# Optimization experiments

Hardware: AMD Instinct MI355X
Metric: run time of the kernel (lower is better)

Reference implementation:

```python
import jax, jax.numpy as jnp
import numpy as np

DIM = 768
HEADS = 12
HEAD_DIM = DIM // HEADS
HIDDEN = 4 * DIM
SCALE = HEAD_DIM ** -0.5
LN_EPS = 1e-5


def _fit_poly_gelu():
    # replicate PolyGELU.__init__: quadratic least-squares fit to exact GELU on [-3,3]
    x = np.linspace(-3.0, 3.0, 10000).astype(np.float32)
    y = np.asarray(jax.nn.gelu(jnp.asarray(x), approximate=False))
    X = np.stack([x ** 2, x, np.ones_like(x)], axis=1)
    c, *_ = np.linalg.lstsq(X, y, rcond=None)
    return c.astype(np.float32)  # [a, b, c]


def setup_inputs() -> dict:
    key = jax.random.key(0)
    ks = jax.random.split(key, 8)
    g = _fit_poly_gelu()
    w = lambda k, shp: (jax.random.normal(k, shp, dtype=jnp.float32) * 0.02)
    return {
        "x": jax.random.normal(ks[0], (4, 2048, DIM), dtype=jnp.float32),
        "ln1_g": jnp.ones((DIM,), jnp.float32),
        "ln1_b": jnp.zeros((DIM,), jnp.float32),
        "ln2_g": jnp.ones((DIM,), jnp.float32),
        "ln2_b": jnp.zeros((DIM,), jnp.float32),
        "qkv_w": w(ks[1], (DIM, 3 * DIM)),   # stored [in, out]
        "qkv_b": jnp.zeros((3 * DIM,), jnp.float32),
        "proj_w": w(ks[2], (DIM, DIM)),
        "proj_b": jnp.zeros((DIM,), jnp.float32),
        "fc1_w": w(ks[3], (DIM, HIDDEN)),
        "fc1_b": jnp.zeros((HIDDEN,), jnp.float32),
        "fc2_w": w(ks[4], (HIDDEN, DIM)),
        "fc2_b": jnp.zeros((DIM,), jnp.float32),
        "attn_a": jnp.float32(0.05),
        "attn_b": jnp.float32(0.5),
        "attn_c": jnp.float32(0.25),
        "gelu_a": jnp.float32(g[0]),
        "gelu_b": jnp.float32(g[1]),
        "gelu_c": jnp.float32(g[2]),
    }


def _layernorm(x, gamma, beta):
    mu = jnp.mean(x, axis=-1, keepdims=True)
    var = jnp.mean(jnp.square(x - mu), axis=-1, keepdims=True)
    return (x - mu) / jnp.sqrt(var + LN_EPS) * gamma + beta


def reference(x, ln1_g, ln1_b, ln2_g, ln2_b, qkv_w, qkv_b, proj_w, proj_b,
              fc1_w, fc1_b, fc2_w, fc2_b, attn_a, attn_b, attn_c,
              gelu_a, gelu_b, gelu_c):
    B, N, C = x.shape
    # --- attention branch ---
    h = _layernorm(x, ln1_g, ln1_b)
    qkv = (h @ qkv_w + qkv_b).reshape(B, N, 3, HEADS, HEAD_DIM)
    q, k, v = (qkv[:, :, i].transpose(0, 2, 1, 3) for i in range(3))  # [B,H,N,D]
    attn = jnp.einsum("bhnd,bhmd->bhnm", q, k) * SCALE
    # poly_normed: quadratic activation, clamp, row-normalize
    attn = attn_a * attn * attn + attn_b * attn + attn_c
    attn = jnp.maximum(attn, 1e-6)
    attn = attn / (jnp.sum(attn, axis=-1, keepdims=True) + 1e-8)
    out = jnp.einsum("bhnm,bhmd->bhnd", attn, v).transpose(0, 2, 1, 3).reshape(B, N, C)
    x = x + (out @ proj_w + proj_b)
    # --- MLP branch with PolyGELU ---
    h = _layernorm(x, ln2_g, ln2_b)
    u = h @ fc1_w + fc1_b
    u = gelu_a * u * u + gelu_b * u + gelu_c
    x = x + (u @ fc2_w + fc2_b)
    return x
```

## Files before the change

### kernel.cpp

```cpp
#include <hip/hip_runtime.h>

typedef __bf16 bf16x8 __attribute__((ext_vector_type(8)));
typedef __bf16 bf16x4 __attribute__((ext_vector_type(4)));
typedef float f32x4 __attribute__((ext_vector_type(4)));

#define LN_EPS 1e-5f

__device__ __forceinline__ void gl2lds16(const void* g, void* l) {
  __builtin_amdgcn_global_load_lds(
      (const __attribute__((address_space(1))) unsigned int*)g,
      (__attribute__((address_space(3))) unsigned int*)l, 16, 0, 0);
}

__global__ __launch_bounds__(256) void transpose_k(const float* __restrict__ in,
                                                   __bf16* __restrict__ out,
                                                   int R, int C) {
  __shared__ __bf16 t[32][33];
  int tx = threadIdx.x & 31, ty = threadIdx.x >> 5;
  int c = blockIdx.x * 32 + tx;
  for (int j = 0; j < 4; j++) {
    int r = blockIdx.y * 32 + ty + j * 8;
    t[ty + j * 8][tx] = (__bf16)in[(size_t)r * C + c];
  }
  __syncthreads();
  int r2 = blockIdx.y * 32 + tx;
  for (int j = 0; j < 4; j++) {
    int c2 = blockIdx.x * 32 + ty + j * 8;
    out[(size_t)c2 * R + r2] = t[tx][ty + j * 8];
  }
}

__global__ __launch_bounds__(256) void transpose_v(const __bf16* __restrict__ qkv,
                                                   __bf16* __restrict__ vt) {
  __shared__ __bf16 t[32][33];
  int bh = blockIdx.z;
  int b = bh / 12, h = bh % 12;
  int n0 = blockIdx.x * 32, d0 = blockIdx.y * 32;
  int tx = threadIdx.x & 31, ty = threadIdx.x >> 5;
  for (int j = 0; j < 4; j++) {
    int n = n0 + ty + j * 8;
    t[ty + j * 8][tx] = qkv[(size_t)(b * 2048 + n) * 2304 + 1536 + h * 64 + d0 + tx];
  }
  __syncthreads();
  for (int j = 0; j < 4; j++) {
    int d = d0 + ty + j * 8;
    vt[((size_t)bh * 64 + d) * 2048 + n0 + tx] = t[tx][ty + j * 8];
  }
}

__global__ __launch_bounds__(256) void ln_kernel(const float* __restrict__ x,
                                                 const float* __restrict__ g,
                                                 const float* __restrict__ bta,
                                                 __bf16* __restrict__ out) {
  int row = blockIdx.x;
  size_t base = (size_t)row * 768;
  int t = threadIdx.x;
  float v[3];
  float s = 0.f, s2 = 0.f;
  for (int k = 0; k < 3; k++) {
    float f = x[base + t + k * 256];
    v[k] = f;
    s += f;
    s2 += f * f;
  }
  for (int m = 1; m < 64; m <<= 1) {
    s += __shfl_xor(s, m, 64);
    s2 += __shfl_xor(s2, m, 64);
  }
  __shared__ float sm[4][2];
  int wid = t >> 6, lane = t & 63;
  if (lane == 0) { sm[wid][0] = s; sm[wid][1] = s2; }
  __syncthreads();
  s = sm[0][0] + sm[1][0] + sm[2][0] + sm[3][0];
  s2 = sm[0][1] + sm[1][1] + sm[2][1] + sm[3][1];
  float mu = s * (1.f / 768.f);
  float var = s2 * (1.f / 768.f) - mu * mu;
  float rstd = rsqrtf(var + LN_EPS);
  for (int k = 0; k < 3; k++) {
    int c = t + k * 256;
    out[base + c] = (__bf16)((v[k] - mu) * rstd * g[c] + bta[c]);
  }
}

template <int NT, int EPI>
__global__ __launch_bounds__(256, (NT == 128 ? 3 : 2))
void gemm_bk64(const __bf16* __restrict__ A, const __bf16* __restrict__ BT,
               const float* __restrict__ bias, const float* __restrict__ res,
               void* __restrict__ outv, int M, int N, int K,
               const float* __restrict__ c0p, const float* __restrict__ c1p,
               const float* __restrict__ c2p) {
  __shared__ __bf16 As[128][64];
  __shared__ __bf16 Bs[NT][64];
  const int tid = threadIdx.x, lane = tid & 63, wid = tid >> 6;
  const int wr = wid >> 1, wc = wid & 1;
  const int mr = lane & 15, quad = lane >> 4;
  const int m0 = blockIdx.y * 128, n0 = blockIdx.x * NT;
  const int swzsrc = (((lane & 7) ^ ((lane >> 3) & 7)) * 8);
  const int srow8 = lane >> 3;
  const int col0 = ((quad ^ (mr & 7)) * 8);
  const int col1 = (((4 + quad) ^ (mr & 7)) * 8);

  f32x4 acc[4][NT / 32] = {};

  for (int k0 = 0; k0 < K; k0 += 64) {
    for (int g = 0; g < 4; g++) {
      int r0 = wid * 32 + g * 8 + srow8;
      gl2lds16(&A[(size_t)(m0 + r0) * K + k0 + swzsrc], &As[r0][(lane & 7) * 8]);
    }
    for (int g = 0; g < NT / 32; g++) {
      int r0 = wid * (NT / 4) + g * 8 + srow8;
      gl2lds16(&BT[(size_t)(n0 + r0) * K + k0 + swzsrc], &Bs[r0][(lane & 7) * 8]);
    }
    __syncthreads();
    for (int kk = 0; kk < 2; kk++) {
      const int ck = kk ? col1 : col0;
      bf16x8 af[4], bfr[NT / 32];
      for (int i = 0; i < 4; i++) af[i] = *(bf16x8*)&As[wr * 64 + i * 16 + mr][ck];
      for (int j = 0; j < NT / 32; j++)
        bfr[j] = *(bf16x8*)&Bs[wc * (NT / 2) + j * 16 + mr][ck];
      for (int i = 0; i < 4; i++)
        for (int j = 0; j < NT / 32; j++)
          acc[i][j] = __builtin_amdgcn_mfma_f32_16x16x32_bf16(af[i], bfr[j], acc[i][j], 0, 0, 0);
    }
    __syncthreads();
  }

  float ga = 0.f, gb = 0.f, gc = 0.f;
  if (EPI == 1) { ga = *c0p; gb = *c1p; gc = *c2p; }

  for (int i = 0; i < 4; i++) {
    for (int j = 0; j < NT / 32; j++) {
      int col = n0 + wc * (NT / 2) + j * 16 + mr;
      float bv = bias[col];
      for (int r = 0; r < 4; r++) {
        int row = m0 + wr * 64 + i * 16 + quad * 4 + r;
        size_t idx = (size_t)row * N + col;
        float c = acc[i][j][r] + bv;
        if (EPI == 0) {
          ((__bf16*)outv)[idx] = (__bf16)c;
        } else if (EPI == 1) {
          float u = (ga * c + gb) * c + gc;
          ((__bf16*)outv)[idx] = (__bf16)u;
        } else {
          ((float*)outv)[idx] = c + res[idx];
        }
      }
    }
  }
}

__global__ __launch_bounds__(256, 3) void attn_poly(const __bf16* __restrict__ qkv,
                                                    const __bf16* __restrict__ vt,
                                                    __bf16* __restrict__ outp,
                                                    const float* __restrict__ ap,
                                                    const float* __restrict__ bp,
                                                    const float* __restrict__ cp) {
  __shared__ __bf16 Ps[4][32][72];
  __shared__ __bf16 Kb[2][64][64];
  __shared__ __bf16 Vb[2][64][64];

  const int tid = threadIdx.x, lane = tid & 63, wid = tid >> 6;
  const int mr = lane & 15, quad = lane >> 4;
  const int q0 = blockIdx.x * 128;
  const int h = blockIdx.y, b = blockIdx.z;
  const int bh = b * 12 + h;
  const size_t baseQ = ((size_t)b * 2048) * 2304 + h * 64;

  const int swzsrc = (((lane & 7) ^ ((lane >> 3) & 7)) * 8);
  const int srow8 = lane >> 3;
  const int colS0 = ((quad ^ (mr & 7)) * 8);
  const int colS1 = (((4 + quad) ^ (mr & 7)) * 8);

  bf16x8 qf[2][2];
  for (int i = 0; i < 2; i++)
    for (int s = 0; s < 2; s++)
      qf[i][s] = *(const bf16x8*)&qkv[baseQ + (size_t)(q0 + wid * 32 + i * 16 + mr) * 2304 +
                                      s * 32 + quad * 8];

  const float a2 = (*ap) * 0.015625f, b2 = (*bp) * 0.125f, cc = *cp;
  f32x4 o_acc[2][4] = {};
  float l_acc[2] = {0.f, 0.f};

  auto stage = [&](int kt, int pb) {
    for (int g = 0; g < 2; g++) {
      int r0 = wid * 16 + g * 8 + srow8;
      gl2lds16(&qkv[baseQ + (size_t)(kt * 64 + r0) * 2304 + 768 + swzsrc],
               &Kb[pb][r0][(lane & 7) * 8]);
      gl2lds16(&vt[((size_t)bh * 64 + r0) * 2048 + kt * 64 + swzsrc],
               &Vb[pb][r0][(lane & 7) * 8]);
    }
  };

  stage(0, 0);
  int pb = 0;
  for (int kt = 0; kt < 32; kt++) {
    __syncthreads();
    if (kt < 31) stage(kt + 1, pb ^ 1);

    f32x4 sacc[2][4] = {};
    for (int j = 0; j < 4; j++) {
      for (int s = 0; s < 2; s++) {
        bf16x8 kf = *(bf16x8*)&Kb[pb][j * 16 + mr][s ? colS1 : colS0];
        for (int i = 0; i < 2; i++)
          sacc[i][j] = __builtin_amdgcn_mfma_f32_16x16x32_bf16(kf, qf[i][s], sacc[i][j], 0, 0, 0);
      }
    }
    for (int i = 0; i < 2; i++) {
      f32x4 racc = {0.f, 0.f, 0.f, 0.f};
      for (int j = 0; j < 4; j++) {
        f32x4 S = sacc[i][j];
        f32x4 p = (a2 * S + b2) * S + cc;
        p[0] = fmaxf(p[0], 1e-6f); p[1] = fmaxf(p[1], 1e-6f);
        p[2] = fmaxf(p[2], 1e-6f); p[3] = fmaxf(p[3], 1e-6f);
        racc += p;
        bf16x4 pk = {(__bf16)p[0], (__bf16)p[1], (__bf16)p[2], (__bf16)p[3]};
        *(bf16x4*)&Ps[wid][i * 16 + mr][j * 16 + quad * 4] = pk;
      }
      float rsum = racc[0] + racc[1] + racc[2] + racc[3];
      rsum += __shfl_xor(rsum, 16, 64);
      rsum += __shfl_xor(rsum, 32, 64);
      l_acc[i] += rsum;
    }

    __asm__ __volatile__("s_waitcnt lgkmcnt(0)" ::: "memory");

    for (int s = 0; s < 2; s++) {
      bf16x8 pf[2];
      for (int i = 0; i < 2; i++)
        pf[i] = *(bf16x8*)&Ps[wid][i * 16 + mr][s * 32 + quad * 8];
      for (int dt = 0; dt < 4; dt++) {
        bf16x8 vf = *(bf16x8*)&Vb[pb][dt * 16 + mr][s ? colS1 : colS0];
        for (int i = 0; i < 2; i++)
          o_acc[i][dt] = __builtin_amdgcn_mfma_f32_16x16x32_bf16(pf[i], vf, o_acc[i][dt], 0, 0, 0);
      }
    }
    __asm__ __volatile__("" ::: "memory");
    pb ^= 1;
  }

  size_t baseO = ((size_t)b * 2048) * 768 + h * 64;
  for (int i = 0; i < 2; i++) {
    float inv[4];
    for (int r = 0; r < 4; r++)
      inv[r] = 1.0f / (__shfl(l_acc[i], quad * 4 + r, 64) + 1e-8f);
    for (int dt = 0; dt < 4; dt++) {
      int q = q0 + wid * 32 + i * 16 + quad * 4;
      for (int r = 0; r < 4; r++)
        outp[baseO + (size_t)(q + r) * 768 + dt * 16 + mr] =
            (__bf16)(o_acc[i][dt][r] * inv[r]);
    }
  }
}

extern "C" void kernel_launch(void* const* d_in, const int* in_sizes, int n_in,
                              void* d_out, int out_size, void* d_ws, size_t ws_size,
                              hipStream_t stream) {
  const float* x     = (const float*)d_in[0];
  const float* ln1g  = (const float*)d_in[1];
  const float* ln1b  = (const float*)d_in[2];
  const float* ln2g  = (const float*)d_in[3];
  const float* ln2b  = (const float*)d_in[4];
  const float* qkvw  = (const float*)d_in[5];
  const float* qkvb  = (const float*)d_in[6];
  const float* projw = (const float*)d_in[7];
  const float* projb = (const float*)d_in[8];
  const float* fc1w  = (const float*)d_in[9];
  const float* fc1b  = (const float*)d_in[10];
  const float* fc2w  = (const float*)d_in[11];
  const float* fc2b  = (const float*)d_in[12];
  const float* attna = (const float*)d_in[13];
  const float* attnb = (const float*)d_in[14];
  const float* attnc = (const float*)d_in[15];
  const float* gelua = (const float*)d_in[16];
  const float* gelub = (const float*)d_in[17];
  const float* geluc = (const float*)d_in[18];

  char* ws = (char*)d_ws;
  __bf16* wT_qkv  = (__bf16*)(ws);
  __bf16* wT_proj = (__bf16*)(ws + 3538944);
  __bf16* wT_fc1  = (__bf16*)(ws + 4718592);
  __bf16* wT_fc2  = (__bf16*)(ws + 9437184);
  __bf16* h       = (__bf16*)(ws + 14155776);
  float*  x1      = (float*)(ws + 26738688);
  __bf16* qkvbuf  = (__bf16*)(ws + 51904512);
  __bf16* u       = (__bf16*)(ws + 51904512);
  __bf16* vtbuf   = (__bf16*)(ws + 89653248);
  float*  outp    = (float*)d_out;

  transpose_k<<<dim3(2304 / 32, 768 / 32), 256, 0, stream>>>(qkvw, wT_qkv, 768, 2304);
  transpose_k<<<dim3(768 / 32, 768 / 32), 256, 0, stream>>>(projw, wT_proj, 768, 768);
  transpose_k<<<dim3(3072 / 32, 768 / 32), 256, 0, stream>>>(fc1w, wT_fc1, 768, 3072);
  transpose_k<<<dim3(768 / 32, 3072 / 32), 256, 0, stream>>>(fc2w, wT_fc2, 3072, 768);

  ln_kernel<<<8192, 256, 0, stream>>>(x, ln1g, ln1b, h);
  gemm_bk64<256, 0><<<dim3(9, 64), 256, 0, stream>>>(h, wT_qkv, qkvb, nullptr, qkvbuf,
                                                     8192, 2304, 768, nullptr, nullptr, nullptr);
  transpose_v<<<dim3(64, 2, 48), 256, 0, stream>>>(qkvbuf, vtbuf);
  attn_poly<<<dim3(16, 12, 4), 256, 0, stream>>>(qkvbuf, vtbuf, h, attna, attnb, attnc);
  gemm_bk64<128, 2><<<dim3(6, 64), 256, 0, stream>>>(h, wT_proj, projb, x, x1,
                                                     8192, 768, 768, nullptr, nullptr, nullptr);
  ln_kernel<<<8192, 256, 0, stream>>>(x1, ln2g, ln2b, h);
  gemm_bk64<256, 1><<<dim3(12, 64), 256, 0, stream>>>(h, wT_fc1, fc1b, nullptr, u,
                                                      8192, 3072, 768, gelua, gelub, geluc);
  gemm_bk64<128, 2><<<dim3(6, 64), 256, 0, stream>>>(u, wT_fc2, fc2b, x1, outp,
                                                     8192, 768, 3072, nullptr, nullptr, nullptr);
}
```

Measured before the change: 411.3 us.

## Double-buffer GEMM LDS tiles with BK32 and smaller output tiles

Replaces the single-buffered BK=64 GEMM with a double-buffered BK=32 kernel that issues the next tile's global-to-LDS loads before computing the current one, leaving one barrier per iteration. Tile shapes shrink (128x128 for qkv/fc1, 64x128 for proj/fc2) and occupancy hints rise to 4 blocks per CU, so more blocks fill the GPU. The aim is to hide load latency and raise occupancy, at the cost of less reuse per tile and more K iterations and barriers. The LDS swizzle is changed to a 4-chunk pattern to match the 32-wide rows.

```diff
diff --git a/kernel.cpp b/kernel.cpp
--- a/kernel.cpp
+++ b/kernel.cpp
@@ -82,58 +82,60 @@
   }
 }
 
-template <int NT, int EPI>
-__global__ __launch_bounds__(256, (NT == 128 ? 3 : 2))
-void gemm_bk64(const __bf16* __restrict__ A, const __bf16* __restrict__ BT,
-               const float* __restrict__ bias, const float* __restrict__ res,
-               void* __restrict__ outv, int M, int N, int K,
-               const float* __restrict__ c0p, const float* __restrict__ c1p,
-               const float* __restrict__ c2p) {
-  __shared__ __bf16 As[128][64];
-  __shared__ __bf16 Bs[NT][64];
+template <int MT, int NT, int EPI>
+__global__ __launch_bounds__(256, 4)
+void gemm_db(const __bf16* __restrict__ A, const __bf16* __restrict__ BT,
+             const float* __restrict__ bias, const float* __restrict__ res,
+             void* __restrict__ outv, int M, int N, int K,
+             const float* __restrict__ c0p, const float* __restrict__ c1p,
+             const float* __restrict__ c2p) {
+  __shared__ __bf16 As[2][MT][32];
+  __shared__ __bf16 Bs[2][NT][32];
+  constexpr int IW = MT / 32, JW = NT / 32;
   const int tid = threadIdx.x, lane = tid & 63, wid = tid >> 6;
   const int wr = wid >> 1, wc = wid & 1;
   const int mr = lane & 15, quad = lane >> 4;
-  const int m0 = blockIdx.y * 128, n0 = blockIdx.x * NT;
-  const int swzsrc = (((lane & 7) ^ ((lane >> 3) & 7)) * 8);
-  const int srow8 = lane >> 3;
-  const int col0 = ((quad ^ (mr & 7)) * 8);
-  const int col1 = (((4 + quad) ^ (mr & 7)) * 8);
-
-  f32x4 acc[4][NT / 32] = {};
-
-  for (int k0 = 0; k0 < K; k0 += 64) {
-    for (int g = 0; g < 4; g++) {
-      int r0 = wid * 32 + g * 8 + srow8;
-      gl2lds16(&A[(size_t)(m0 + r0) * K + k0 + swzsrc], &As[r0][(lane & 7) * 8]);
-    }
-    for (int g = 0; g < NT / 32; g++) {
-      int r0 = wid * (NT / 4) + g * 8 + srow8;
-      gl2lds16(&BT[(size_t)(n0 + r0) * K + k0 + swzsrc], &Bs[r0][(lane & 7) * 8]);
-    }
+  const int m0 = blockIdx.y * MT, n0 = blockIdx.x * NT;
+  const int swzsrc = (((lane & 3) ^ ((lane >> 2) & 3)) * 8);
+  const int srow = lane >> 2;
+  const int ck = ((quad ^ (mr & 3)) * 8);
+
+  f32x4 acc[IW][JW] = {};
+
+  auto stage = [&](int k0, int pb) {
+    for (int g = 0; g < MT / 64; g++) {
+      int r0 = wid * (MT / 4) + g * 16 + srow;
+      gl2lds16(&A[(size_t)(m0 + r0) * K + k0 + swzsrc], &As[pb][r0][(lane & 3) * 8]);
+    }
+    for (int g = 0; g < NT / 64; g++) {
+      int r0 = wid * (NT / 4) + g * 16 + srow;
+      gl2lds16(&BT[(size_t)(n0 + r0) * K + k0 + swzsrc], &Bs[pb][r0][(lane & 3) * 8]);
+    }
+  };
+
+  stage(0, 0);
+  int pb = 0;
+  for (int k0 = 0; k0 < K; k0 += 32) {
     __syncthreads();
-    for (int kk = 0; kk < 2; kk++) {
-      const int ck = kk ? col1 : col0;
-      bf16x8 af[4], bfr[NT / 32];
-      for (int i = 0; i < 4; i++) af[i] = *(bf16x8*)&As[wr * 64 + i * 16 + mr][ck];
-      for (int j = 0; j < NT / 32; j++)
-        bfr[j] = *(bf16x8*)&Bs[wc * (NT / 2) + j * 16 + mr][ck];
-      for (int i = 0; i < 4; i++)
-        for (int j = 0; j < NT / 32; j++)
-          acc[i][j] = __builtin_amdgcn_mfma_f32_16x16x32_bf16(af[i], bfr[j], acc[i][j], 0, 0, 0);
-    }
-    __syncthreads();
+    if (k0 + 32 < K) stage(k0 + 32, pb ^ 1);
+    bf16x8 af[IW], bfr[JW];
+    for (int i = 0; i < IW; i++) af[i] = *(bf16x8*)&As[pb][wr * (MT / 2) + i * 16 + mr][ck];
+    for (int j = 0; j < JW; j++) bfr[j] = *(bf16x8*)&Bs[pb][wc * (NT / 2) + j * 16 + mr][ck];
+    for (int i = 0; i < IW; i++)
+      for (int j = 0; j < JW; j++)
+        acc[i][j] = __builtin_amdgcn_mfma_f32_16x16x32_bf16(af[i], bfr[j], acc[i][j], 0, 0, 0);
+    pb ^= 1;
   }
 
   float ga = 0.f, gb = 0.f, gc = 0.f;
   if (EPI == 1) { ga = *c0p; gb = *c1p; gc = *c2p; }
 
-  for (int i = 0; i < 4; i++) {
-    for (int j = 0; j < NT / 32; j++) {
+  for (int i = 0; i < IW; i++) {
+    for (int j = 0; j < JW; j++) {
       int col = n0 + wc * (NT / 2) + j * 16 + mr;
       float bv = bias[col];
       for (int r = 0; r < 4; r++) {
-        int row = m0 + wr * 64 + i * 16 + quad * 4 + r;
+        int row = m0 + wr * (MT / 2) + i * 16 + quad * 4 + r;
         size_t idx = (size_t)row * N + col;
         float c = acc[i][j][r] + bv;
         if (EPI == 0) {
@@ -293,15 +295,15 @@
   transpose_k<<<dim3(768 / 32, 3072 / 32), 256, 0, stream>>>(fc2w, wT_fc2, 3072, 768);
 
   ln_kernel<<<8192, 256, 0, stream>>>(x, ln1g, ln1b, h);
-  gemm_bk64<256, 0><<<dim3(9, 64), 256, 0, stream>>>(h, wT_qkv, qkvb, nullptr, qkvbuf,
-                                                     8192, 2304, 768, nullptr, nullptr, nullptr);
+  gemm_db<128, 128, 0><<<dim3(18, 64), 256, 0, stream>>>(h, wT_qkv, qkvb, nullptr, qkvbuf,
+                                                         8192, 2304, 768, nullptr, nullptr, nullptr);
   transpose_v<<<dim3(64, 2, 48), 256, 0, stream>>>(qkvbuf, vtbuf);
   attn_poly<<<dim3(16, 12, 4), 256, 0, stream>>>(qkvbuf, vtbuf, h, attna, attnb, attnc);
-  gemm_bk64<128, 2><<<dim3(6, 64), 256, 0, stream>>>(h, wT_proj, projb, x, x1,
-                                                     8192, 768, 768, nullptr, nullptr, nullptr);
+  gemm_db<64, 128, 2><<<dim3(6, 128), 256, 0, stream>>>(h, wT_proj, projb, x, x1,
+                                                        8192, 768, 768, nullptr, nullptr, nullptr);
   ln_kernel<<<8192, 256, 0, stream>>>(x1, ln2g, ln2b, h);
-  gemm_bk64<256, 1><<<dim3(12, 64), 256, 0, stream>>>(h, wT_fc1, fc1b, nullptr, u,
-                                                      8192, 3072, 768, gelua, gelub, geluc);
-  gemm_bk64<128, 2><<<dim3(6, 64), 256, 0, stream>>>(u, wT_fc2, fc2b, x1, outp,
-                                                     8192, 768, 3072, nullptr, nullptr, nullptr);
-}
+  gemm_db<128, 128, 1><<<dim3(24, 64), 256, 0, stream>>>(h, wT_fc1, fc1b, nullptr, u,
+                                                         8192, 3072, 768, gelua, gelub, geluc);
+  gemm_db<64, 128, 2><<<dim3(6, 128), 256, 0, stream>>>(u, wT_fc2, fc2b, x1, outp,
+                                                        8192, 768, 3072, nullptr, nullptr, nullptr);
+}
```

Result: slower. 424.8 us (+3.3%).
